# Kernel optimization log

Measured on AMD Instinct MI355X. Metric: run time of the kernel, lower is better.

## Reference

```python
import jax, jax.numpy as jnp
import numpy as np

N = 50000    # num nodes
E = 800000   # num edges
B = 256      # num graphs
AD, BD = 39, 10          # atom / bond feature dims
H, HEADS, HD, L, TD = 128, 4, 32, 3, 128  # hidden, heads, head_dim, layers, time_dim
BN_EPS = 1e-5


def setup_inputs() -> dict:
    key = jax.random.key(0)
    ks = jax.random.split(key, 24)
    g = lambda i, shape: jax.random.normal(ks[i], shape, dtype=jnp.float32) * 0.05
    return {
        "x": jax.random.normal(ks[0], (N, AD), dtype=jnp.float32),
        "edge_index": jax.random.randint(ks[1], (2, E), 0, N),
        "edge_attr": jax.random.normal(ks[2], (E, BD), dtype=jnp.float32),
        "batch": jnp.sort(jax.random.randint(ks[3], (N,), 0, B)),
        "t": jax.random.randint(ks[4], (B,), 0, 1000),
        "atom_W": g(5, (AD, H)), "atom_b": jnp.zeros((H,), jnp.float32),
        "bond_W": g(6, (BD, H)), "bond_b": jnp.zeros((H,), jnp.float32),
        "lin_W": g(7, (L, H, H)), "edge_W": g(8, (L, H, H)),
        "att_src": g(9, (L, HEADS, HD)), "att_dst": g(10, (L, HEADS, HD)),
        "att_edge": g(11, (L, HEADS, HD)), "conv_b": jnp.zeros((L, H), jnp.float32),
        "bn_gamma": jnp.ones((L, H), jnp.float32), "bn_beta": jnp.zeros((L, H), jnp.float32),
        "out_W": g(12, (H, H)), "out_b": jnp.zeros((H,), jnp.float32),
        "time_W1": g(13, (TD, H)), "time_b1": jnp.zeros((H,), jnp.float32),
        "time_W2": g(14, (H, H)), "time_b2": jnp.zeros((H,), jnp.float32),
        "pool_W1": g(15, (H, H)), "pool_b1": jnp.zeros((H,), jnp.float32),
        "pool_W2": g(16, (H, H)), "pool_b2": jnp.zeros((H,), jnp.float32),
        "np_W1": g(17, (2 * H, H)), "np_b1": jnp.zeros((H,), jnp.float32),
        "np_W2": g(18, (H, H)), "np_b2": jnp.zeros((H,), jnp.float32),
        "np_W3": g(19, (H, AD)), "np_b3": jnp.zeros((AD,), jnp.float32),
    }


def _time_embedding(tf):
    half = TD // 2
    freqs = jnp.exp(jnp.arange(half, dtype=jnp.float32) * (-np.log(10000.0) / (half - 1)))
    e = tf[:, None] * freqs[None, :]
    return jnp.concatenate([jnp.sin(e), jnp.cos(e)], axis=-1)


def _gat_layer(h, e_emb, src, dst, W, We, a_src, a_dst, a_edge, bias):
    # PyG GATConv: shared lin for src/dst, edge features modulate attention only.
    xh = (h @ W).reshape(N, HEADS, HD)
    eh = (e_emb @ We).reshape(E, HEADS, HD)
    s_src = jnp.sum(xh * a_src, axis=-1)    # [N, HEADS]
    s_dst = jnp.sum(xh * a_dst, axis=-1)    # [N, HEADS]
    s_edge = jnp.sum(eh * a_edge, axis=-1)  # [E, HEADS]
    alpha = jax.nn.leaky_relu(s_src[src] + s_dst[dst] + s_edge, 0.2)  # [E, HEADS]
    amax = jax.ops.segment_max(alpha, dst, num_segments=N)
    amax = jnp.where(jnp.isfinite(amax), amax, 0.0)
    ea = jnp.exp(alpha - amax[dst])
    denom = jax.ops.segment_sum(ea, dst, num_segments=N)
    w = ea / (denom[dst] + 1e-16)           # segment softmax over incoming edges
    msg = xh[src] * w[:, :, None]           # [E, HEADS, HD]
    return jax.ops.segment_sum(msg, dst, num_segments=N).reshape(N, H) + bias


def reference(x, edge_index, edge_attr, batch, t,
              atom_W, atom_b, bond_W, bond_b,
              lin_W, edge_W, att_src, att_dst, att_edge, conv_b, bn_gamma, bn_beta,
              out_W, out_b, time_W1, time_b1, time_W2, time_b2,
              pool_W1, pool_b1, pool_W2, pool_b2,
              np_W1, np_b1, np_W2, np_b2, np_W3, np_b3):
    src, dst = edge_index[0], edge_index[1]
    # time conditioning
    t_emb = _time_embedding(t.astype(jnp.float32))
    t_emb = jax.nn.silu(t_emb @ time_W1 + time_b1) @ time_W2 + time_b2  # [B, H]
    # GNN backbone
    h = x @ atom_W + atom_b
    e_emb = edge_attr @ bond_W + bond_b
    for i in range(L):
        h_in = h
        h = _gat_layer(h, e_emb, src, dst, lin_W[i], edge_W[i],
                       att_src[i], att_dst[i], att_edge[i], conv_b[i])
        mu = h.mean(axis=0)
        var = h.var(axis=0)
        h = (h - mu) / jnp.sqrt(var + BN_EPS) * bn_gamma[i] + bn_beta[i]
        h = jax.nn.relu(h)
        h = h + h_in  # residual (dropout is eval-mode identity)
    node_features = h @ out_W + out_b  # [N, H]
    # graph mean pool + pooling MLP
    counts = jnp.clip(jax.ops.segment_sum(jnp.ones((N,), h.dtype), batch, num_segments=B), 1.0, None)
    graph = jax.ops.segment_sum(node_features, batch, num_segments=B) / counts[:, None]
    graph = jax.nn.silu(graph @ pool_W1 + pool_b1) @ pool_W2 + pool_b2  # [B, H]
    tg = t_emb + graph
    # per-node noise prediction
    z = jnp.concatenate([node_features, tg[batch]], axis=-1)  # [N, 2H]
    z = jax.nn.silu(z @ np_W1 + np_b1)
    z = jax.nn.silu(z @ np_W2 + np_b2)
    return z @ np_W3 + np_b3  # [N, AD]
```

## Files before the change

kernel.cpp:

```cpp
#include <hip/hip_runtime.h>
#include <hip/hip_fp16.h>
#include <math.h>

#define N_NODES 50000
#define N_EDGES 800000
#define NB 256
#define AD 39
#define BD 10
#define H 128
#define HEADS 4
#define HD 32
#define LAYERS 3
#define TD 128
#define NBUCK 196
#define EPB 4096

typedef _Float16 f16x8 __attribute__((ext_vector_type(8)));
typedef float f32x4 __attribute__((ext_vector_type(4)));

__device__ __forceinline__ float silu_f(float x) { return x / (1.f + __expf(-x)); }

__device__ __forceinline__ void fma_rank1(float acc[8][4], float4 aL, float4 aH, float4 w)
{
    float ar[8] = {aL.x, aL.y, aL.z, aL.w, aH.x, aH.y, aH.z, aH.w};
    float wr[4] = {w.x, w.y, w.z, w.w};
#pragma unroll
    for (int r = 0; r < 8; r++)
#pragma unroll
        for (int j = 0; j < 4; j++) acc[r][j] += ar[r] * wr[j];
}

template<int KT>
__global__ __launch_bounds__(256) void gemm128(
    const float* __restrict__ A, const float* __restrict__ W,
    const float* __restrict__ bias, float* __restrict__ out,
    int Nrows, int ldw)
{
    __shared__ float As[KT * 68];
    const int tid = threadIdx.x;
    const int rowBase = blockIdx.x * 64;

    for (int idx = tid; idx < 64 * KT; idx += 256) {
        int row = idx / KT;
        int k = idx - row * KT;
        int n = rowBase + row;
        As[k * 68 + row] = (n < Nrows) ? A[(size_t)n * KT + k] : 0.f;
    }
    __syncthreads();

    const int c0 = (tid & 31) * 4;
    const int n0 = (tid >> 5) * 8;

    float acc[8][4];
#pragma unroll
    for (int r = 0; r < 8; r++)
#pragma unroll
        for (int j = 0; j < 4; j++) acc[r][j] = 0.f;

    const float* wp = W + c0;
    int k = 0;
    for (; k + 4 <= KT; k += 4) {
        float4 w0 = *(const float4*)&wp[(size_t)(k + 0) * ldw];
        float4 w1 = *(const float4*)&wp[(size_t)(k + 1) * ldw];
        float4 w2 = *(const float4*)&wp[(size_t)(k + 2) * ldw];
        float4 w3 = *(const float4*)&wp[(size_t)(k + 3) * ldw];
        float4 aL0 = *(const float4*)&As[(k + 0) * 68 + n0];
        float4 aH0 = *(const float4*)&As[(k + 0) * 68 + n0 + 4];
        float4 aL1 = *(const float4*)&As[(k + 1) * 68 + n0];
        float4 aH1 = *(const float4*)&As[(k + 1) * 68 + n0 + 4];
        float4 aL2 = *(const float4*)&As[(k + 2) * 68 + n0];
        float4 aH2 = *(const float4*)&As[(k + 2) * 68 + n0 + 4];
        float4 aL3 = *(const float4*)&As[(k + 3) * 68 + n0];
        float4 aH3 = *(const float4*)&As[(k + 3) * 68 + n0 + 4];
        fma_rank1(acc, aL0, aH0, w0);
        fma_rank1(acc, aL1, aH1, w1);
        fma_rank1(acc, aL2, aH2, w2);
        fma_rank1(acc, aL3, aH3, w3);
    }
    for (; k < KT; ++k) {
        float4 w0 = *(const float4*)&wp[(size_t)k * ldw];
        float4 aL = *(const float4*)&As[k * 68 + n0];
        float4 aH = *(const float4*)&As[k * 68 + n0 + 4];
        fma_rank1(acc, aL, aH, w0);
    }

    float4 bv = make_float4(0.f, 0.f, 0.f, 0.f);
    if (bias) bv = *(const float4*)&bias[c0];

#pragma unroll
    for (int r = 0; r < 8; r++) {
        int n = rowBase + n0 + r;
        if (n >= Nrows) break;
        float4 o;
        o.x = acc[r][0] + bv.x;
        o.y = acc[r][1] + bv.y;
        o.z = acc[r][2] + bv.z;
        o.w = acc[r][3] + bv.w;
        *(float4*)&out[(size_t)n * H + c0] = o;
    }
}

__global__ __launch_bounds__(256) void convert_w_frags(
    const float* __restrict__ lin_W, const float* __restrict__ out_W,
    __half* __restrict__ w16)
{
    int tid = blockIdx.x * 256 + threadIdx.x;
    if (tid >= 4 * H * H) return;
    int mat = tid >> 14;
    int rem = tid & 16383;
    int k = rem >> 7;
    int n = rem & 127;
    const float* src = (mat < 3) ? (lin_W + (size_t)mat * H * H) : out_W;
    float v = src[(size_t)k * H + n];
    int ks = k >> 5, kr = k & 31;
    int lane = ((kr >> 3) << 4) | (n & 15);
    int j = kr & 7;
    int nb = n >> 4;
    w16[(size_t)mat * 16384 + (((ks * 8 + nb) * 64 + lane) << 3) + j] = __float2half(v);
}

__global__ __launch_bounds__(256) void convert_np_frags(
    const float* __restrict__ npW1, const float* __restrict__ npW2,
    const float* __restrict__ npW3, __half* __restrict__ wnp)
{
    int tid = blockIdx.x * 256 + threadIdx.x;
    const int TOT12 = 2 * H * H;
    if (tid < TOT12) {
        int mat = tid >> 14;
        int rem = tid & 16383;
        int k = rem >> 7;
        int n = rem & 127;
        const float* src = mat ? npW2 : npW1;
        float v = src[(size_t)k * H + n];
        int ks = k >> 5, kr = k & 31;
        int lane = ((kr >> 3) << 4) | (n & 15);
        int j = kr & 7;
        int nb = n >> 4;
        wnp[(size_t)mat * 16384 + (((ks * 8 + nb) * 64 + lane) << 3) + j] = __float2half(v);
    } else {
        int r = tid - TOT12;
        if (r >= H * 48) return;
        int k = r / 48;
        int n = r - k * 48;
        float v = (n < AD) ? npW3[(size_t)k * AD + n] : 0.f;
        int ks = k >> 5, kr = k & 31;
        int lane = ((kr >> 3) << 4) | (n & 15);
        int j = kr & 7;
        int nb = n >> 4;
        wnp[32768 + (((ks * 3 + nb) * 64 + lane) << 3) + j] = __float2half(v);
    }
}

__global__ __launch_bounds__(256) void gemm_mfma_bn(
    const float* __restrict__ A,
    const __half* __restrict__ agg, const float* __restrict__ scale,
    const float* __restrict__ shift, float* __restrict__ hio,
    const __half* __restrict__ wfrag, const float* __restrict__ bias,
    float* __restrict__ out32, __half* __restrict__ out16,
    const float* __restrict__ attS, const float* __restrict__ attD,
    float* __restrict__ sS, float* __restrict__ sD, int Nrows)
{
    __shared__ __half Ah[64 * 136];
    const int tid = threadIdx.x;
    const int rowBase = blockIdx.x * 64;

    for (int idx = tid; idx < 64 * 32; idx += 256) {
        int row = idx >> 5;
        int kq = (idx & 31) * 4;
        int n = rowBase + row;
        float4 v = make_float4(0.f, 0.f, 0.f, 0.f);
        if (n < Nrows) {
            if (agg) {
                uint2 u = *(const uint2*)&agg[(size_t)n * H + kq];
                float2 lo = __half22float2(*(__half2*)&u.x);
                float2 hi = __half22float2(*(__half2*)&u.y);
                float4 sc = *(const float4*)&scale[kq];
                float4 sh = *(const float4*)&shift[kq];
                float4 hv = *(const float4*)&hio[(size_t)n * H + kq];
                v.x = fmaxf(lo.x * sc.x + sh.x, 0.f) + hv.x;
                v.y = fmaxf(lo.y * sc.y + sh.y, 0.f) + hv.y;
                v.z = fmaxf(hi.x * sc.z + sh.z, 0.f) + hv.z;
                v.w = fmaxf(hi.y * sc.w + sh.w, 0.f) + hv.w;
                *(float4*)&hio[(size_t)n * H + kq] = v;
            } else {
                v = *(const float4*)&A[(size_t)n * H + kq];
            }
        }
        __half2 a = __floats2half2_rn(v.x, v.y);
        __half2 b = __floats2half2_rn(v.z, v.w);
        *(uint2*)&Ah[row * 136 + kq] = make_uint2(*(unsigned*)&a, *(unsigned*)&b);
    }
    __syncthreads();

    const int wave = tid >> 6;
    const int lane = tid & 63;
    const int lrow = lane & 15;
    const int lgrp = lane >> 4;

    f16x8 bf[4][2];
#pragma unroll
    for (int ks = 0; ks < 4; ks++)
#pragma unroll
        for (int nt = 0; nt < 2; nt++) {
            int nb = wave * 2 + nt;
            bf[ks][nt] = *(const f16x8*)&wfrag[(((ks * 8 + nb) * 64 + lane) << 3)];
        }

    f32x4 acc[4][2];
#pragma unroll
    for (int mt = 0; mt < 4; mt++)
#pragma unroll
        for (int nt = 0; nt < 2; nt++) acc[mt][nt] = (f32x4){0.f, 0.f, 0.f, 0.f};

#pragma unroll
    for (int ks = 0; ks < 4; ks++) {
#pragma unroll
        for (int mt = 0; mt < 4; mt++) {
            f16x8 af = *(const f16x8*)&Ah[(mt * 16 + lrow) * 136 + ks * 32 + lgrp * 8];
            acc[mt][0] = __builtin_amdgcn_mfma_f32_16x16x32_f16(af, bf[ks][0], acc[mt][0], 0, 0, 0);
            acc[mt][1] = __builtin_amdgcn_mfma_f32_16x16x32_f16(af, bf[ks][1], acc[mt][1], 0, 0, 0);
        }
    }

    const int col0 = wave * 32 + lrow;
    const int col1 = col0 + 16;
    float b0 = bias ? bias[col0] : 0.f;
    float b1 = bias ? bias[col1] : 0.f;
    float aS0 = 0.f, aS1 = 0.f, aD0 = 0.f, aD1 = 0.f;
    if (sS) {
        aS0 = attS[col0]; aS1 = attS[col1];
        aD0 = attD[col0]; aD1 = attD[col1];
    }

#pragma unroll
    for (int mt = 0; mt < 4; mt++) {
#pragma unroll
        for (int reg = 0; reg < 4; reg++) {
            int row = rowBase + mt * 16 + lgrp * 4 + reg;
            float v0 = acc[mt][0][reg] + b0;
            float v1 = acc[mt][1][reg] + b1;
            if (row < Nrows) {
                if (out16) {
                    out16[(size_t)row * H + col0] = __float2half(v0);
                    out16[(size_t)row * H + col1] = __float2half(v1);
                } else {
                    out32[(size_t)row * H + col0] = v0;
                    out32[(size_t)row * H + col1] = v1;
                }
            }
            if (sS) {
                float ps = v0 * aS0 + v1 * aS1;
                float pd = v0 * aD0 + v1 * aD1;
#pragma unroll
                for (int off = 8; off >= 1; off >>= 1) {
                    ps += __shfl_xor(ps, off, 16);
                    pd += __shfl_xor(pd, off, 16);
                }
                if (lrow == 0 && row < Nrows) {
                    sS[row * 4 + wave] = ps;
                    sD[row * 4 + wave] = pd;
                }
            }
        }
    }
}

__global__ __launch_bounds__(256) void np_fused_mfma(
    const float* __restrict__ nf, const int* __restrict__ batch,
    const float* __restrict__ tgW, const __half* __restrict__ wnp,
    const float* __restrict__ npb2, const float* __restrict__ npb3,
    float* __restrict__ out, int Nrows)
{
    __shared__ __half Ah[64 * 136];
    const int tid = threadIdx.x;
    const int rowBase = blockIdx.x * 64;

    for (int idx = tid; idx < 64 * 32; idx += 256) {
        int row = idx >> 5;
        int kq = (idx & 31) * 4;
        int n = rowBase + row;
        float4 v = make_float4(0.f, 0.f, 0.f, 0.f);
        if (n < Nrows) v = *(const float4*)&nf[(size_t)n * H + kq];
        __half2 a = __floats2half2_rn(v.x, v.y);
        __half2 b = __floats2half2_rn(v.z, v.w);
        *(uint2*)&Ah[row * 136 + kq] = make_uint2(*(unsigned*)&a, *(unsigned*)&b);
    }
    __syncthreads();

    const int wave = tid >> 6;
    const int lane = tid & 63;
    const int lrow = lane & 15;
    const int lgrp = lane >> 4;

    f32x4 acc[4][2];

    {
        f16x8 bf[4][2];
#pragma unroll
        for (int ks = 0; ks < 4; ks++)
#pragma unroll
            for (int nt = 0; nt < 2; nt++) {
                int nb = wave * 2 + nt;
                bf[ks][nt] = *(const f16x8*)&wnp[(((ks * 8 + nb) * 64 + lane) << 3)];
            }
#pragma unroll
        for (int mt = 0; mt < 4; mt++)
#pragma unroll
            for (int nt = 0; nt < 2; nt++) acc[mt][nt] = (f32x4){0.f, 0.f, 0.f, 0.f};
#pragma unroll
        for (int ks = 0; ks < 4; ks++) {
#pragma unroll
            for (int mt = 0; mt < 4; mt++) {
                f16x8 af = *(const f16x8*)&Ah[(mt * 16 + lrow) * 136 + ks * 32 + lgrp * 8];
                acc[mt][0] = __builtin_amdgcn_mfma_f32_16x16x32_f16(af, bf[ks][0], acc[mt][0], 0, 0, 0);
                acc[mt][1] = __builtin_amdgcn_mfma_f32_16x16x32_f16(af, bf[ks][1], acc[mt][1], 0, 0, 0);
            }
        }
    }
    __syncthreads();

#pragma unroll
    for (int mt = 0; mt < 4; mt++) {
#pragma unroll
        for (int nt = 0; nt < 2; nt++) {
            int col = wave * 32 + nt * 16 + lrow;
#pragma unroll
            for (int reg = 0; reg < 4; reg++) {
                int row = mt * 16 + lgrp * 4 + reg;
                int n = rowBase + row;
                float v = acc[mt][nt][reg];
                if (n < Nrows) v += tgW[(size_t)batch[n] * H + col];
                Ah[row * 136 + col] = __float2half(silu_f(v));
            }
        }
    }
    __syncthreads();

    {
        const __half* w2 = wnp + 16384;
        f16x8 bf[4][2];
#pragma unroll
        for (int ks = 0; ks < 4; ks++)
#pragma unroll
            for (int nt = 0; nt < 2; nt++) {
                int nb = wave * 2 + nt;
                bf[ks][nt] = *(const f16x8*)&w2[(((ks * 8 + nb) * 64 + lane) << 3)];
            }
#pragma unroll
        for (int mt = 0; mt < 4; mt++)
#pragma unroll
            for (int nt = 0; nt < 2; nt++) acc[mt][nt] = (f32x4){0.f, 0.f, 0.f, 0.f};
#pragma unroll
        for (int ks = 0; ks < 4; ks++) {
#pragma unroll
            for (int mt = 0; mt < 4; mt++) {
                f16x8 af = *(const f16x8*)&Ah[(mt * 16 + lrow) * 136 + ks * 32 + lgrp * 8];
                acc[mt][0] = __builtin_amdgcn_mfma_f32_16x16x32_f16(af, bf[ks][0], acc[mt][0], 0, 0, 0);
                acc[mt][1] = __builtin_amdgcn_mfma_f32_16x16x32_f16(af, bf[ks][1], acc[mt][1], 0, 0, 0);
            }
        }
    }
    __syncthreads();

#pragma unroll
    for (int mt = 0; mt < 4; mt++) {
#pragma unroll
        for (int nt = 0; nt < 2; nt++) {
            int col = wave * 32 + nt * 16 + lrow;
            float b2 = npb2[col];
#pragma unroll
            for (int reg = 0; reg < 4; reg++) {
                int row = mt * 16 + lgrp * 4 + reg;
                Ah[row * 136 + col] = __float2half(silu_f(acc[mt][nt][reg] + b2));
            }
        }
    }
    __syncthreads();

    {
        const __half* w3 = wnp + 32768;
        f32x4 acc3[3];
#pragma unroll
        for (int nt = 0; nt < 3; nt++) acc3[nt] = (f32x4){0.f, 0.f, 0.f, 0.f};
#pragma unroll
        for (int ks = 0; ks < 4; ks++) {
            f16x8 af = *(const f16x8*)&Ah[(wave * 16 + lrow) * 136 + ks * 32 + lgrp * 8];
#pragma unroll
            for (int nt = 0; nt < 3; nt++) {
                f16x8 bf = *(const f16x8*)&w3[(((ks * 3 + nt) * 64 + lane) << 3)];
                acc3[nt] = __builtin_amdgcn_mfma_f32_16x16x32_f16(af, bf, acc3[nt], 0, 0, 0);
            }
        }
#pragma unroll
        for (int nt = 0; nt < 3; nt++) {
            int col = nt * 16 + lrow;
            if (col < AD) {
                float b3 = npb3[col];
#pragma unroll
                for (int reg = 0; reg < 4; reg++) {
                    int row = rowBase + wave * 16 + lgrp * 4 + reg;
                    if (row < Nrows) out[(size_t)row * AD + col] = acc3[nt][reg] + b3;
                }
            }
        }
    }
}

__global__ __launch_bounds__(256) void precompute_small(
    const float* __restrict__ edge_W, const float* __restrict__ att_edge,
    const float* __restrict__ bond_W, const float* __restrict__ bond_b,
    float* __restrict__ mc)
{
    __shared__ float bl[LAYERS][H][4];
    int tid = threadIdx.x;
    for (int task = tid; task < LAYERS * H; task += 256) {
        int l = task / H, k = task % H;
#pragma unroll
        for (int hh = 0; hh < 4; hh++) {
            float s = 0.f;
            for (int d = 0; d < HD; d++)
                s += edge_W[(size_t)l * H * H + k * H + hh * HD + d] *
                     att_edge[l * H + hh * HD + d];
            bl[l][k][hh] = s;
        }
    }
    __syncthreads();
    if (tid < LAYERS * BD * 4) {
        int l = tid / (BD * 4), r = tid % (BD * 4), j = r / 4, hh = r % 4;
        float s = 0.f;
        for (int k = 0; k < H; k++) s += bond_W[j * H + k] * bl[l][k][hh];
        mc[l * 44 + j * 4 + hh] = s;
    }
    if (tid >= 128 && tid < 128 + LAYERS * 4) {
        int r = tid - 128, l = r / 4, hh = r % 4;
        float s = 0.f;
        for (int k = 0; k < H; k++) s += bond_b[k] * bl[l][k][hh];
        mc[l * 44 + 40 + hh] = s;
    }
}

__global__ __launch_bounds__(128) void time_embed(
    const int* __restrict__ t,
    const float* __restrict__ W1, const float* __restrict__ b1,
    const float* __restrict__ W2, const float* __restrict__ b2,
    float* __restrict__ t_emb)
{
    int g = blockIdx.x, c = threadIdx.x;
    float tf = (float)t[g];
    __shared__ float emb[TD], z[H];
    int k = c & 63;
    float f = __expf(-9.210340371976184f * (float)k / 63.0f);
    float e = tf * f;
    emb[c] = (c < 64) ? sinf(e) : cosf(e);
    __syncthreads();
    float a1 = b1[c];
    for (int kk = 0; kk < TD; kk++) a1 += emb[kk] * W1[kk * H + c];
    z[c] = silu_f(a1);
    __syncthreads();
    float a2 = b2[c];
    for (int kk = 0; kk < H; kk++) a2 += z[kk] * W2[kk * H + c];
    t_emb[g * H + c] = a2;
}

__global__ __launch_bounds__(256) void hist_dst(const int* __restrict__ edge_index,
                                                int* __restrict__ deg)
{
    int e = blockIdx.x * 256 + threadIdx.x;
    if (e < N_EDGES) atomicAdd(&deg[edge_index[N_EDGES + e]], 1);
}

__global__ __launch_bounds__(320) void gptr_bsearch(const int* __restrict__ batch,
                                                    int* __restrict__ gptr)
{
    int g = threadIdx.x;
    if (g > NB) return;
    int lo = 0, hi = N_NODES;
    while (lo < hi) {
        int mid = (lo + hi) >> 1;
        if (batch[mid] < g) lo = mid + 1; else hi = mid;
    }
    gptr[g] = lo;
}

__global__ __launch_bounds__(256) void scan_part(const int* __restrict__ cnt,
                                                 int* __restrict__ bsum, int n)
{
    int tid = threadIdx.x;
    int i0 = blockIdx.x * 1024 + tid * 4;
    int s = 0;
#pragma unroll
    for (int j = 0; j < 4; j++) if (i0 + j < n) s += cnt[i0 + j];
    __shared__ int red[256];
    red[tid] = s;
    __syncthreads();
    for (int off = 128; off >= 1; off >>= 1) {
        if (tid < off) red[tid] += red[tid + off];
        __syncthreads();
    }
    if (tid == 0) bsum[blockIdx.x] = red[0];
}

__global__ __launch_bounds__(256) void scan_tops(const int* __restrict__ bsum,
                                                 int* __restrict__ boff, int G,
                                                 int* __restrict__ total)
{
    int tid = threadIdx.x;
    int v = (tid < G) ? bsum[tid] : 0;
    __shared__ int ps[256];
    ps[tid] = v;
    __syncthreads();
    for (int off = 1; off < 256; off <<= 1) {
        int t = (tid >= off) ? ps[tid - off] : 0;
        __syncthreads();
        ps[tid] += t;
        __syncthreads();
    }
    if (tid < G) boff[tid] = ps[tid] - v;
    if (tid == 255) *total = ps[255];
}

__global__ __launch_bounds__(256) void scan_final(const int* __restrict__ cnt,
                                                  const int* __restrict__ boff,
                                                  int* __restrict__ ptr, int n)
{
    int tid = threadIdx.x;
    int i0 = blockIdx.x * 1024 + tid * 4;
    int v[4];
#pragma unroll
    for (int j = 0; j < 4; j++) v[j] = (i0 + j < n) ? cnt[i0 + j] : 0;
    int s = v[0] + v[1] + v[2] + v[3];
    __shared__ int ps[256];
    ps[tid] = s;
    __syncthreads();
    for (int off = 1; off < 256; off <<= 1) {
        int t = (tid >= off) ? ps[tid - off] : 0;
        __syncthreads();
        ps[tid] += t;
        __syncthreads();
    }
    int run = boff[blockIdx.x] + ps[tid] - s;
#pragma unroll
    for (int j = 0; j < 4; j++) {
        if (i0 + j < n) { ptr[i0 + j] = run; run += v[j]; }
    }
}

__global__ __launch_bounds__(256) void init_gcur(const int* __restrict__ csr_ptr,
                                                 int* __restrict__ gcur)
{
    int b = threadIdx.x;
    if (b < NBUCK) gcur[b] = csr_ptr[min(b << 8, N_NODES)];
}

__global__ __launch_bounds__(256) void bucket_scatter_a(
    const int* __restrict__ edge_index, int* __restrict__ gcur,
    int4* __restrict__ tmp)
{
    __shared__ int cnt[NBUCK], cbase[NBUCK], cur[NBUCK];
    const int tid = threadIdx.x;
    const int e0 = blockIdx.x * EPB;
    for (int i = tid; i < NBUCK; i += 256) { cnt[i] = 0; cur[i] = 0; }
    __syncthreads();
    for (int i = 0; i < EPB; i += 256) {
        int e = e0 + i + tid;
        if (e < N_EDGES) atomicAdd(&cnt[edge_index[N_EDGES + e] >> 8], 1);
    }
    __syncthreads();
    for (int i = tid; i < NBUCK; i += 256)
        if (cnt[i] > 0) cbase[i] = atomicAdd(&gcur[i], cnt[i]);
    __syncthreads();
    for (int i = 0; i < EPB; i += 256) {
        int e = e0 + i + tid;
        if (e < N_EDGES) {
            int s = edge_index[e];
            int d = edge_index[N_EDGES + e];
            int b = d >> 8;
            int off = atomicAdd(&cur[b], 1);
            tmp[cbase[b] + off] = make_int4(s, e, d, 0);
        }
    }
}

__global__ __launch_bounds__(256) void bucket_scatter_b(
    const int4* __restrict__ tmp, const int* __restrict__ csr_ptr,
    int2* __restrict__ csr_se)
{
    __shared__ int lcur[256];
    const int b = blockIdx.x;
    const int n0 = b << 8;
    const int tid = threadIdx.x;
    lcur[tid] = 0;
    __syncthreads();
    int start = csr_ptr[n0];
    int end   = csr_ptr[min(n0 + 256, N_NODES)];
    for (int p = start + tid; p < end; p += 256) {
        int4 q = tmp[p];
        int pos = atomicAdd(&lcur[q.z - n0], 1);
        csr_se[csr_ptr[q.z] + pos] = make_int2(q.x, q.y);
    }
}

__global__ __launch_bounds__(256) void se3_pre(
    const int2* __restrict__ csr_se, const float* __restrict__ edge_attr,
    const float* __restrict__ mc, __half* __restrict__ se3)
{
    __shared__ float Ml[LAYERS * 44];
    int tid = threadIdx.x;
    if (tid < LAYERS * 44) Ml[tid] = mc[tid];
    __syncthreads();
    int p = blockIdx.x * 256 + tid;
    if (p >= N_EDGES) return;
    int e = csr_se[p].y;
    float ea[BD];
    const float* eap = &edge_attr[(size_t)e * BD];
#pragma unroll
    for (int j = 0; j < BD; j++) ea[j] = eap[j];
#pragma unroll
    for (int l = 0; l < LAYERS; l++) {
        const float* M = &Ml[l * 44];
        float s0 = M[40], s1 = M[41], s2 = M[42], s3 = M[43];
#pragma unroll
        for (int j = 0; j < BD; j++) {
            float x = ea[j];
            s0 += x * M[j * 4 + 0]; s1 += x * M[j * 4 + 1];
            s2 += x * M[j * 4 + 2]; s3 += x * M[j * 4 + 3];
        }
        __half2 h01 = __floats2half2_rn(s0, s1);
        __half2 h23 = __floats2half2_rn(s2, s3);
        uint2 u = make_uint2(*(const unsigned*)&h01, *(const unsigned*)&h23);
        *(uint2*)&se3[((size_t)l * N_EDGES + p) * 4] = u;
    }
}

__global__ __launch_bounds__(256) void gat_agg_full(
    const __half* __restrict__ xh16, const __half* __restrict__ se3l,
    const float* __restrict__ sS,
    const int* __restrict__ csr_ptr, const int2* __restrict__ csr_se,
    const float* __restrict__ sD, const float* __restrict__ conv_b_l,
    __half* __restrict__ agg)
{
    int n = (blockIdx.x * 256 + threadIdx.x) >> 6;
    if (n >= N_NODES) return;
    int lane = threadIdx.x & 63;
    int c0 = lane * 2;
    int hd = lane >> 4;
    int start = csr_ptr[n], end = csr_ptr[n + 1];
    float sDn = sD[n * 4 + hd];

    float m_run = -1e30f, d_run = 0.f;
    float acc0 = 0.f, acc1 = 0.f;

    for (int base = start; base < end; base += 64) {
        int cnt = min(64, end - base);
        int s_l = (lane < cnt) ? csr_se[base + lane].x : 0;

        float a_t[4], e_t[4];
        float m_blk = -1e30f;
#pragma unroll
        for (int t = 0; t < 4; t++) {
            int i = (lane & 15) + t * 16;
            float a = -1e30f;
            if (i < cnt) {
                int src = __shfl(s_l, i);
                a = sS[src * 4 + hd] +
                    __half2float(se3l[(size_t)(base + i) * 4 + hd]) + sDn;
                a = (a >= 0.f) ? a : 0.2f * a;
            }
            a_t[t] = a;
            m_blk = fmaxf(m_blk, a);
        }
#pragma unroll
        for (int off = 8; off >= 1; off >>= 1)
            m_blk = fmaxf(m_blk, __shfl_xor(m_blk, off, 16));
        float m_new = fmaxf(m_run, m_blk);
        float rescale = __expf(m_run - m_new);
        float dsum = 0.f;
#pragma unroll
        for (int t = 0; t < 4; t++) {
            e_t[t] = __expf(a_t[t] - m_new);
            dsum += e_t[t];
        }
#pragma unroll
        for (int off = 8; off >= 1; off >>= 1)
            dsum += __shfl_xor(dsum, off, 16);
        d_run = d_run * rescale + dsum;
        acc0 *= rescale;
        acc1 *= rescale;

        int srcb = lane & 48;
#pragma unroll
        for (int t = 0; t < 4; t++) {
            int rem = cnt - t * 16;
            if (rem <= 0) break;
            int lim = min(16, (rem + 3) & ~3);
            for (int i2 = 0; i2 < lim; i2 += 4) {
                int i = t * 16 + i2;
                int s0 = __shfl(s_l, i + 0), s1 = __shfl(s_l, i + 1);
                int s2 = __shfl(s_l, i + 2), s3 = __shfl(s_l, i + 3);
                float w0 = __shfl(e_t[t], srcb | (i2 + 0));
                float w1 = __shfl(e_t[t], srcb | (i2 + 1));
                float w2 = __shfl(e_t[t], srcb | (i2 + 2));
                float w3 = __shfl(e_t[t], srcb | (i2 + 3));
                float2 x0 = __half22float2(*(const __half2*)&xh16[(size_t)s0 * H + c0]);
                float2 x1 = __half22float2(*(const __half2*)&xh16[(size_t)s1 * H + c0]);
                float2 x2 = __half22float2(*(const __half2*)&xh16[(size_t)s2 * H + c0]);
                float2 x3 = __half22float2(*(const __half2*)&xh16[(size_t)s3 * H + c0]);
                acc0 += x0.x * w0 + x1.x * w1 + x2.x * w2 + x3.x * w3;
                acc1 += x0.y * w0 + x1.y * w1 + x2.y * w2 + x3.y * w3;
            }
        }
        m_run = m_new;
    }
    float inv = 1.f / (d_run + 1e-16f);
    __half2 o = __floats2half2_rn(acc0 * inv + conv_b_l[c0],
                                  acc1 * inv + conv_b_l[c0 + 1]);
    *(__half2*)&agg[(size_t)n * H + c0] = o;
}

__global__ __launch_bounds__(256) void bn_partial_f(const __half* __restrict__ agg,
                                                    float* __restrict__ part)
{
    const int PER = (N_NODES + 511) / 512;
    __shared__ float red[2][8][128];
    int b = blockIdx.x;
    int cg = threadIdx.x & 31;
    int rs = threadIdx.x >> 5;
    int c4 = cg * 4;
    int s = b * PER, e = min(N_NODES, s + PER);
    float s0 = 0.f, s1 = 0.f, s2 = 0.f, s3 = 0.f;
    float q0 = 0.f, q1 = 0.f, q2 = 0.f, q3 = 0.f;
    for (int n = s + rs; n < e; n += 8) {
        uint2 u = *(const uint2*)&agg[(size_t)n * H + c4];
        float2 lo = __half22float2(*(__half2*)&u.x);
        float2 hi = __half22float2(*(__half2*)&u.y);
        s0 += lo.x; q0 += lo.x * lo.x;
        s1 += lo.y; q1 += lo.y * lo.y;
        s2 += hi.x; q2 += hi.x * hi.x;
        s3 += hi.y; q3 += hi.y * hi.y;
    }
    *(float4*)&red[0][rs][c4] = make_float4(s0, s1, s2, s3);
    *(float4*)&red[1][rs][c4] = make_float4(q0, q1, q2, q3);
    __syncthreads();
    if (threadIdx.x < 128) {
        int c = threadIdx.x;
        float sum = 0.f, sq = 0.f;
#pragma unroll
        for (int r = 0; r < 8; r++) { sum += red[0][r][c]; sq += red[1][r][c]; }
        part[b * H + c] = sum;
        part[512 * H + b * H + c] = sq;
    }
}

__global__ __launch_bounds__(256) void bn_finish_f(const float* __restrict__ part,
                                                   const float* __restrict__ gamma,
                                                   const float* __restrict__ beta,
                                                   float* __restrict__ scale,
                                                   float* __restrict__ shift)
{
    __shared__ double red[2][2][128];
    int c = threadIdx.x & 127;
    int g = threadIdx.x >> 7;
    double s = 0.0, q = 0.0;
    for (int b = g * 256; b < (g + 1) * 256; b++) {
        s += (double)part[b * H + c];
        q += (double)part[512 * H + b * H + c];
    }
    red[0][g][c] = s;
    red[1][g][c] = q;
    __syncthreads();
    if (g == 0) {
        s = red[0][0][c] + red[0][1][c];
        q = red[1][0][c] + red[1][1][c];
        float mu = (float)(s / N_NODES);
        float var = (float)(q / N_NODES) - mu * mu;
        float rstd = rsqrtf(var + 1e-5f);
        float sc = gamma[c] * rstd;
        scale[c] = sc;
        shift[c] = beta[c] - mu * sc;
    }
}

__global__ __launch_bounds__(128) void pool_partial(
    const float* __restrict__ nf, const int* __restrict__ gptr,
    float* __restrict__ pprt)
{
    int g = blockIdx.x >> 2;
    int q = blockIdx.x & 3;
    int c = threadIdx.x;
    int s = gptr[g], e = gptr[g + 1];
    int qlen = (e - s + 3) >> 2;
    int qs = s + q * qlen;
    int qe = min(e, qs + qlen);
    float sum = 0.f;
    for (int n = qs; n < qe; n++) sum += nf[(size_t)n * H + c];
    pprt[((size_t)g * 4 + q) * H + c] = sum;
}

__global__ __launch_bounds__(512) void graph_head_mlp(
    const int* __restrict__ gptr, const float* __restrict__ pprt,
    const float* __restrict__ t_emb,
    const float* __restrict__ pW1, const float* __restrict__ pb1,
    const float* __restrict__ pW2, const float* __restrict__ pb2,
    const float* __restrict__ npW1, const float* __restrict__ npb1,
    float* __restrict__ tgW)
{
    int g = blockIdx.x;
    int c = threadIdx.x & 127;
    int q = threadIdx.x >> 7;
    __shared__ float row[H], z[H];
    __shared__ float red[4][H];

    int s = gptr[g], e = gptr[g + 1];
    float cf = (e - s > 0) ? (float)(e - s) : 1.f;
    if (q == 0) {
        row[c] = (pprt[((size_t)g * 4 + 0) * H + c] +
                  pprt[((size_t)g * 4 + 1) * H + c] +
                  pprt[((size_t)g * 4 + 2) * H + c] +
                  pprt[((size_t)g * 4 + 3) * H + c]) / cf;
    }
    __syncthreads();

    float p = 0.f;
#pragma unroll 8
    for (int k = q * 32; k < q * 32 + 32; k++) p += row[k] * pW1[k * H + c];
    red[q][c] = p;
    __syncthreads();
    if (q == 0) z[c] = silu_f(red[0][c] + red[1][c] + red[2][c] + red[3][c] + pb1[c]);
    __syncthreads();

    p = 0.f;
#pragma unroll 8
    for (int k = q * 32; k < q * 32 + 32; k++) p += z[k] * pW2[k * H + c];
    red[q][c] = p;
    __syncthreads();
    if (q == 0) row[c] = red[0][c] + red[1][c] + red[2][c] + red[3][c] + pb2[c]
                         + t_emb[g * H + c];
    __syncthreads();

    p = 0.f;
#pragma unroll 8
    for (int k = q * 32; k < q * 32 + 32; k++)
        p += row[k] * npW1[(size_t)(128 + k) * H + c];
    red[q][c] = p;
    __syncthreads();
    if (q == 0) tgW[g * H + c] = red[0][c] + red[1][c] + red[2][c] + red[3][c] + npb1[c];
}

extern "C" void kernel_launch(void* const* d_in, const int* in_sizes, int n_in,
                              void* d_out, int out_size, void* d_ws, size_t ws_size,
                              hipStream_t stream)
{
    const float* x          = (const float*)d_in[0];
    const int*   edge_index = (const int*)d_in[1];
    const float* edge_attr  = (const float*)d_in[2];
    const int*   batch      = (const int*)d_in[3];
    const int*   t          = (const int*)d_in[4];
    const float* atom_W     = (const float*)d_in[5];
    const float* atom_b     = (const float*)d_in[6];
    const float* bond_W     = (const float*)d_in[7];
    const float* bond_b     = (const float*)d_in[8];
    const float* lin_W      = (const float*)d_in[9];
    const float* edge_W     = (const float*)d_in[10];
    const float* att_src    = (const float*)d_in[11];
    const float* att_dst    = (const float*)d_in[12];
    const float* att_edge   = (const float*)d_in[13];
    const float* conv_b     = (const float*)d_in[14];
    const float* bn_gamma   = (const float*)d_in[15];
    const float* bn_beta    = (const float*)d_in[16];
    const float* out_W      = (const float*)d_in[17];
    const float* out_b      = (const float*)d_in[18];
    const float* time_W1    = (const float*)d_in[19];
    const float* time_b1    = (const float*)d_in[20];
    const float* time_W2    = (const float*)d_in[21];
    const float* time_b2    = (const float*)d_in[22];
    const float* pool_W1    = (const float*)d_in[23];
    const float* pool_b1    = (const float*)d_in[24];
    const float* pool_W2    = (const float*)d_in[25];
    const float* pool_b2    = (const float*)d_in[26];
    const float* np_W1      = (const float*)d_in[27];
    const float* np_b1      = (const float*)d_in[28];
    const float* np_W2      = (const float*)d_in[29];
    const float* np_b2      = (const float*)d_in[30];
    const float* np_W3      = (const float*)d_in[31];
    const float* np_b3      = (const float*)d_in[32];

    const size_t OFF_H     = 0;
    const size_t OFF_XH    = 6400000;
    const size_t OFF_AGG   = 12800000;
    const size_t OFF_SD    = 17600000;
    const size_t OFF_TEMB  = 17800000;
    const size_t OFF_TGW   = 17832768;
    const size_t OFF_MC    = 17865536;
    const size_t OFF_BNSC  = 17865792;
    const size_t OFF_BNSH  = 17865920;
    const size_t OFF_PART  = 17866048;
    const size_t OFF_SE3   = 17898816;
    const size_t REQ_FLOATS = 22698816;
    const size_t REQ_BYTES  = REQ_FLOATS * 4;

    if (ws_size < REQ_BYTES) {
        hipMemsetAsync(d_out, 0, (size_t)out_size * sizeof(float), stream);
        return;
    }

    float* fws    = (float*)d_ws;
    float* h      = fws + OFF_H;
    float* xh     = fws + OFF_XH;
    __half* xh16  = (__half*)(fws + OFF_XH);
    int4*  etmp   = (int4*)(fws + OFF_XH);
    __half* agg   = (__half*)(fws + OFF_AGG);
    float* sD     = fws + OFF_SD;
    float* t_emb  = fws + OFF_TEMB;
    float* tgW    = fws + OFF_TGW;
    float* mc     = fws + OFF_MC;
    float* bnsc   = fws + OFF_BNSC;
    float* bnsh   = fws + OFF_BNSH;
    float* part   = fws + OFF_PART;
    float* pprt   = fws + OFF_AGG;
    __half* wnp   = (__half*)part;
    __half* se3   = (__half*)(fws + OFF_SE3);

    int* ib       = (int*)d_out;
    int* csr_ptr  = ib;
    int2* csr_se  = (int2*)(ib + 50016);
    int* deg      = ib + 1650016;
    int* gcur     = deg;
    int* gptr     = ib + 1700032;
    int* bsum     = ib + 1700292;
    int* boff     = ib + 1700356;
    float* sS     = (float*)d_out + 1700420;
    float* bnpart = sS;
    __half* w16   = (__half*)((float*)d_out + 1900420);

    hipMemsetAsync(deg, 0, N_NODES * sizeof(int), stream);

    precompute_small<<<1, 256, 0, stream>>>(edge_W, att_edge, bond_W, bond_b, mc);
    time_embed<<<NB, 128, 0, stream>>>(t, time_W1, time_b1, time_W2, time_b2, t_emb);
    gptr_bsearch<<<1, 320, 0, stream>>>(batch, gptr);
    convert_w_frags<<<(4 * H * H + 255) / 256, 256, 0, stream>>>(lin_W, out_W, w16);

    hist_dst<<<(N_EDGES + 255) / 256, 256, 0, stream>>>(edge_index, deg);

    const int GSN = (N_NODES + 1023) / 1024;
    scan_part<<<GSN, 256, 0, stream>>>(deg, bsum, N_NODES);
    scan_tops<<<1, 256, 0, stream>>>(bsum, boff, GSN, &csr_ptr[N_NODES]);
    scan_final<<<GSN, 256, 0, stream>>>(deg, boff, csr_ptr, N_NODES);

    init_gcur<<<1, 256, 0, stream>>>(csr_ptr, gcur);
    bucket_scatter_a<<<(N_EDGES + EPB - 1) / EPB, 256, 0, stream>>>(
        edge_index, gcur, etmp);
    bucket_scatter_b<<<NBUCK, 256, 0, stream>>>(etmp, csr_ptr, csr_se);

    const int GB = (N_NODES + 63) / 64;
    const int GE = (N_EDGES + 255) / 256;

    se3_pre<<<GE, 256, 0, stream>>>(csr_se, edge_attr, mc, se3);

    gemm128<AD><<<GB, 256, 0, stream>>>(x, atom_W, atom_b, h, N_NODES, H);

    for (int l = 0; l < LAYERS; l++) {
        gemm_mfma_bn<<<GB, 256, 0, stream>>>(
            (l == 0) ? h : nullptr,
            (l == 0) ? nullptr : agg, bnsc, bnsh, h,
            w16 + (size_t)l * 16384, nullptr,
            nullptr, xh16,
            att_src + l * H, att_dst + l * H, sS, sD, N_NODES);
        gat_agg_full<<<N_NODES / 4, 256, 0, stream>>>(
            xh16, se3 + (size_t)l * N_EDGES * 4, sS,
            csr_ptr, csr_se, sD, conv_b + l * H, agg);
        bn_partial_f<<<512, 256, 0, stream>>>(agg, bnpart);
        bn_finish_f<<<1, 256, 0, stream>>>(bnpart, bn_gamma + l * H,
                                           bn_beta + l * H, bnsc, bnsh);
    }

    convert_np_frags<<<(2 * H * H + H * 48 + 255) / 256, 256, 0, stream>>>(
        np_W1, np_W2, np_W3, wnp);

    gemm_mfma_bn<<<GB, 256, 0, stream>>>(
        nullptr, agg, bnsc, bnsh, h,
        w16 + (size_t)3 * 16384, out_b,
        xh, nullptr,
        nullptr, nullptr, nullptr, nullptr, N_NODES);

    pool_partial<<<NB * 4, 128, 0, stream>>>(xh, gptr, pprt);
    graph_head_mlp<<<NB, 512, 0, stream>>>(gptr, pprt, t_emb, pool_W1, pool_b1,
                                           pool_W2, pool_b2, np_W1, np_b1, tgW);

    np_fused_mfma<<<GB, 256, 0, stream>>>(xh, batch, tgW, wnp, np_b2, np_b3,
                                          (float*)d_out, N_NODES);
}
```

Before: 441.8 us.

## Drop online-softmax max tracking in GAT aggregation and merge setup kernels

The GAT aggregation kernel no longer tracks a running maximum or rescales its accumulators. It exponentiates the LeakyReLU scores directly and sums them, and it pre-shifts source indices so the row offset is computed once per edge. Several small setup launches are also merged: precompute, time embedding and graph-pointer search go into one kernel, the two weight-fragment conversions go into another, and `gcur` initialisation is folded into `scan_final`. The cost is numerical safety: without max subtraction, large attention logits could overflow `exp`. Converting the np weights earlier also assumes their buffer is not overwritten during the layers.

```diff
diff --git a/kernel.cpp b/kernel.cpp
--- a/kernel.cpp
+++ b/kernel.cpp
@@ -100,34 +100,31 @@
     }
 }
 
-__global__ __launch_bounds__(256) void convert_w_frags(
+__global__ __launch_bounds__(256) void convert_all(
     const float* __restrict__ lin_W, const float* __restrict__ out_W,
-    __half* __restrict__ w16)
+    const float* __restrict__ npW1, const float* __restrict__ npW2,
+    const float* __restrict__ npW3,
+    __half* __restrict__ w16, __half* __restrict__ wnp)
 {
     int tid = blockIdx.x * 256 + threadIdx.x;
-    if (tid >= 4 * H * H) return;
-    int mat = tid >> 14;
-    int rem = tid & 16383;
-    int k = rem >> 7;
-    int n = rem & 127;
-    const float* src = (mat < 3) ? (lin_W + (size_t)mat * H * H) : out_W;
-    float v = src[(size_t)k * H + n];
-    int ks = k >> 5, kr = k & 31;
-    int lane = ((kr >> 3) << 4) | (n & 15);
-    int j = kr & 7;
-    int nb = n >> 4;
-    w16[(size_t)mat * 16384 + (((ks * 8 + nb) * 64 + lane) << 3) + j] = __float2half(v);
-}
-
-__global__ __launch_bounds__(256) void convert_np_frags(
-    const float* __restrict__ npW1, const float* __restrict__ npW2,
-    const float* __restrict__ npW3, __half* __restrict__ wnp)
-{
-    int tid = blockIdx.x * 256 + threadIdx.x;
-    const int TOT12 = 2 * H * H;
-    if (tid < TOT12) {
+    if (tid < 4 * H * H) {
         int mat = tid >> 14;
         int rem = tid & 16383;
+        int k = rem >> 7;
+        int n = rem & 127;
+        const float* src = (mat < 3) ? (lin_W + (size_t)mat * H * H) : out_W;
+        float v = src[(size_t)k * H + n];
+        int ks = k >> 5, kr = k & 31;
+        int lane = ((kr >> 3) << 4) | (n & 15);
+        int j = kr & 7;
+        int nb = n >> 4;
+        w16[(size_t)mat * 16384 + (((ks * 8 + nb) * 64 + lane) << 3) + j] = __float2half(v);
+        return;
+    }
+    int r = tid - 4 * H * H;
+    if (r < 2 * H * H) {
+        int mat = r >> 14;
+        int rem = r & 16383;
         int k = rem >> 7;
         int n = rem & 127;
         const float* src = mat ? npW2 : npW1;
@@ -137,17 +134,84 @@
         int j = kr & 7;
         int nb = n >> 4;
         wnp[(size_t)mat * 16384 + (((ks * 8 + nb) * 64 + lane) << 3) + j] = __float2half(v);
+        return;
+    }
+    r -= 2 * H * H;
+    if (r >= H * 48) return;
+    int k = r / 48;
+    int n = r - k * 48;
+    float v = (n < AD) ? npW3[(size_t)k * AD + n] : 0.f;
+    int ks = k >> 5, kr = k & 31;
+    int lane = ((kr >> 3) << 4) | (n & 15);
+    int j = kr & 7;
+    int nb = n >> 4;
+    wnp[32768 + (((ks * 3 + nb) * 64 + lane) << 3) + j] = __float2half(v);
+}
+
+__global__ __launch_bounds__(256) void setup_misc(
+    const float* __restrict__ edge_W, const float* __restrict__ att_edge,
+    const float* __restrict__ bond_W, const float* __restrict__ bond_b,
+    float* __restrict__ mc,
+    const int* __restrict__ batch, int* __restrict__ gptr,
+    const int* __restrict__ t,
+    const float* __restrict__ W1, const float* __restrict__ b1,
+    const float* __restrict__ W2, const float* __restrict__ b2,
+    float* __restrict__ t_emb)
+{
+    const int b = blockIdx.x;
+    const int tid = threadIdx.x;
+    if (b == 0) {
+        __shared__ float bl[LAYERS][H][4];
+        for (int task = tid; task < LAYERS * H; task += 256) {
+            int l = task / H, k = task % H;
+#pragma unroll
+            for (int hh = 0; hh < 4; hh++) {
+                float s = 0.f;
+                for (int d = 0; d < HD; d++)
+                    s += edge_W[(size_t)l * H * H + k * H + hh * HD + d] *
+                         att_edge[l * H + hh * HD + d];
+                bl[l][k][hh] = s;
+            }
+        }
+        __syncthreads();
+        if (tid < LAYERS * BD * 4) {
+            int l = tid / (BD * 4), r = tid % (BD * 4), j = r / 4, hh = r % 4;
+            float s = 0.f;
+            for (int k = 0; k < H; k++) s += bond_W[j * H + k] * bl[l][k][hh];
+            mc[l * 44 + j * 4 + hh] = s;
+        }
+        if (tid >= 128 && tid < 128 + LAYERS * 4) {
+            int r = tid - 128, l = r / 4, hh = r % 4;
+            float s = 0.f;
+            for (int k = 0; k < H; k++) s += bond_b[k] * bl[l][k][hh];
+            mc[l * 44 + 40 + hh] = s;
+        }
+    } else if (b == 1) {
+        for (int g = tid; g <= NB; g += 256) {
+            int lo = 0, hi = N_NODES;
+            while (lo < hi) {
+                int mid = (lo + hi) >> 1;
+                if (batch[mid] < g) lo = mid + 1; else hi = mid;
+            }
+            gptr[g] = lo;
+        }
     } else {
-        int r = tid - TOT12;
-        if (r >= H * 48) return;
-        int k = r / 48;
-        int n = r - k * 48;
-        float v = (n < AD) ? npW3[(size_t)k * AD + n] : 0.f;
-        int ks = k >> 5, kr = k & 31;
-        int lane = ((kr >> 3) << 4) | (n & 15);
-        int j = kr & 7;
-        int nb = n >> 4;
-        wnp[32768 + (((ks * 3 + nb) * 64 + lane) << 3) + j] = __float2half(v);
+        int g = b - 2;
+        int c = tid & 127;
+        float tf = (float)t[g];
+        __shared__ float emb[TD], z[H];
+        int k = c & 63;
+        float f = __expf(-9.210340371976184f * (float)k / 63.0f);
+        float e = tf * f;
+        emb[c] = (c < 64) ? sinf(e) : cosf(e);
+        __syncthreads();
+        float a1 = b1[c];
+        for (int kk = 0; kk < TD; kk++) a1 += emb[kk] * W1[kk * H + c];
+        z[c] = silu_f(a1);
+        __syncthreads();
+        float a2 = b2[c];
+        for (int kk = 0; kk < H; kk++) a2 += z[kk] * W2[kk * H + c];
+        t_emb[g * H + c] = a2;
     }
 }
 
@@ -406,80 +470,11 @@
     }
 }
 
-__global__ __launch_bounds__(256) void precompute_small(
-    const float* __restrict__ edge_W, const float* __restrict__ att_edge,
-    const float* __restrict__ bond_W, const float* __restrict__ bond_b,
-    float* __restrict__ mc)
-{
-    __shared__ float bl[LAYERS][H][4];
-    int tid = threadIdx.x;
-    for (int task = tid; task < LAYERS * H; task += 256) {
-        int l = task / H, k = task % H;
-#pragma unroll
-        for (int hh = 0; hh < 4; hh++) {
-            float s = 0.f;
-            for (int d = 0; d < HD; d++)
-                s += edge_W[(size_t)l * H * H + k * H + hh * HD + d] *
-                     att_edge[l * H + hh * HD + d];
-            bl[l][k][hh] = s;
-        }
-    }
-    __syncthreads();
-    if (tid < LAYERS * BD * 4) {
-        int l = tid / (BD * 4), r = tid % (BD * 4), j = r / 4, hh = r % 4;
-        float s = 0.f;
-        for (int k = 0; k < H; k++) s += bond_W[j * H + k] * bl[l][k][hh];
-        mc[l * 44 + j * 4 + hh] = s;
-    }
-    if (tid >= 128 && tid < 128 + LAYERS * 4) {
-        int r = tid - 128, l = r / 4, hh = r % 4;
-        float s = 0.f;
-        for (int k = 0; k < H; k++) s += bond_b[k] * bl[l][k][hh];
-        mc[l * 44 + 40 + hh] = s;
-    }
-}
-
-__global__ __launch_bounds__(128) void time_embed(
-    const int* __restrict__ t,
-    const float* __restrict__ W1, const float* __restrict__ b1,
-    const float* __restrict__ W2, const float* __restrict__ b2,
-    float* __restrict__ t_emb)
-{
-    int g = blockIdx.x, c = threadIdx.x;
-    float tf = (float)t[g];
-    __shared__ float emb[TD], z[H];
-    int k = c & 63;
-    float f = __expf(-9.210340371976184f * (float)k / 63.0f);
-    float e = tf * f;
-    emb[c] = (c < 64) ? sinf(e) : cosf(e);
-    __syncthreads();
-    float a1 = b1[c];
-    for (int kk = 0; kk < TD; kk++) a1 += emb[kk] * W1[kk * H + c];
-    z[c] = silu_f(a1);
-    __syncthreads();
-    float a2 = b2[c];
-    for (int kk = 0; kk < H; kk++) a2 += z[kk] * W2[kk * H + c];
-    t_emb[g * H + c] = a2;
-}
-
 __global__ __launch_bounds__(256) void hist_dst(const int* __restrict__ edge_index,
                                                 int* __restrict__ deg)
 {
     int e = blockIdx.x * 256 + threadIdx.x;
     if (e < N_EDGES) atomicAdd(&deg[edge_index[N_EDGES + e]], 1);
-}
-
-__global__ __launch_bounds__(320) void gptr_bsearch(const int* __restrict__ batch,
-                                                    int* __restrict__ gptr)
-{
-    int g = threadIdx.x;
-    if (g > NB) return;
-    int lo = 0, hi = N_NODES;
-    while (lo < hi) {
-        int mid = (lo + hi) >> 1;
-        if (batch[mid] < g) lo = mid + 1; else hi = mid;
-    }
-    gptr[g] = lo;
 }
 
 __global__ __launch_bounds__(256) void scan_part(const int* __restrict__ cnt,
@@ -521,7 +516,8 @@
 
 __global__ __launch_bounds__(256) void scan_final(const int* __restrict__ cnt,
                                                   const int* __restrict__ boff,
-                                                  int* __restrict__ ptr, int n)
+                                                  int* __restrict__ ptr,
+                                                  int* __restrict__ gcur, int n)
 {
     int tid = threadIdx.x;
     int i0 = blockIdx.x * 1024 + tid * 4;
@@ -539,17 +535,11 @@
         __syncthreads();
     }
     int run = boff[blockIdx.x] + ps[tid] - s;
+    if ((i0 & 255) == 0 && (i0 >> 8) < NBUCK && i0 < n) gcur[i0 >> 8] = run;
 #pragma unroll
     for (int j = 0; j < 4; j++) {
         if (i0 + j < n) { ptr[i0 + j] = run; run += v[j]; }
     }
-}
-
-__global__ __launch_bounds__(256) void init_gcur(const int* __restrict__ csr_ptr,
-                                                 int* __restrict__ gcur)
-{
-    int b = threadIdx.x;
-    if (b < NBUCK) gcur[b] = csr_ptr[min(b << 8, N_NODES)];
 }
 
 __global__ __launch_bounds__(256) void bucket_scatter_a(
@@ -647,45 +637,33 @@
     int start = csr_ptr[n], end = csr_ptr[n + 1];
     float sDn = sD[n * 4 + hd];
 
-    float m_run = -1e30f, d_run = 0.f;
+    float d_run = 0.f;
     float acc0 = 0.f, acc1 = 0.f;
 
     for (int base = start; base < end; base += 64) {
         int cnt = min(64, end - base);
-        int s_l = (lane < cnt) ? csr_se[base + lane].x : 0;
-
-        float a_t[4], e_t[4];
-        float m_blk = -1e30f;
+        int s_l = (lane < cnt) ? (csr_se[base + lane].x << 7) : 0;
+
+        float e_t[4];
+        float dsum = 0.f;
 #pragma unroll
         for (int t = 0; t < 4; t++) {
             int i = (lane & 15) + t * 16;
-            float a = -1e30f;
+            float e = 0.f;
             if (i < cnt) {
-                int src = __shfl(s_l, i);
-                a = sS[src * 4 + hd] +
+                int src7 = __shfl(s_l, i);
+                float a = sS[(src7 >> 5) + hd] +
                     __half2float(se3l[(size_t)(base + i) * 4 + hd]) + sDn;
                 a = (a >= 0.f) ? a : 0.2f * a;
-            }
-            a_t[t] = a;
-            m_blk = fmaxf(m_blk, a);
-        }
-#pragma unroll
-        for (int off = 8; off >= 1; off >>= 1)
-            m_blk = fmaxf(m_blk, __shfl_xor(m_blk, off, 16));
-        float m_new = fmaxf(m_run, m_blk);
-        float rescale = __expf(m_run - m_new);
-        float dsum = 0.f;
-#pragma unroll
-        for (int t = 0; t < 4; t++) {
-            e_t[t] = __expf(a_t[t] - m_new);
-            dsum += e_t[t];
+                e = __expf(a);
+            }
+            e_t[t] = e;
+            dsum += e;
         }
 #pragma unroll
         for (int off = 8; off >= 1; off >>= 1)
             dsum += __shfl_xor(dsum, off, 16);
-        d_run = d_run * rescale + dsum;
-        acc0 *= rescale;
-        acc1 *= rescale;
+        d_run += dsum;
 
         int srcb = lane & 48;
 #pragma unroll
@@ -701,15 +679,14 @@
                 float w1 = __shfl(e_t[t], srcb | (i2 + 1));
                 float w2 = __shfl(e_t[t], srcb | (i2 + 2));
                 float w3 = __shfl(e_t[t], srcb | (i2 + 3));
-                float2 x0 = __half22float2(*(const __half2*)&xh16[(size_t)s0 * H + c0]);
-                float2 x1 = __half22float2(*(const __half2*)&xh16[(size_t)s1 * H + c0]);
-                float2 x2 = __half22float2(*(const __half2*)&xh16[(size_t)s2 * H + c0]);
-                float2 x3 = __half22float2(*(const __half2*)&xh16[(size_t)s3 * H + c0]);
+                float2 x0 = __half22float2(*(const __half2*)&xh16[s0 + c0]);
+                float2 x1 = __half22float2(*(const __half2*)&xh16[s1 + c0]);
+                float2 x2 = __half22float2(*(const __half2*)&xh16[s2 + c0]);
+                float2 x3 = __half22float2(*(const __half2*)&xh16[s3 + c0]);
                 acc0 += x0.x * w0 + x1.x * w1 + x2.x * w2 + x3.x * w3;
                 acc1 += x0.y * w0 + x1.y * w1 + x2.y * w2 + x3.y * w3;
             }
         }
-        m_run = m_new;
     }
     float inv = 1.f / (d_run + 1e-16f);
     __half2 o = __floats2half2_rn(acc0 * inv + conv_b_l[c0],
@@ -924,29 +901,30 @@
     int* csr_ptr  = ib;
     int2* csr_se  = (int2*)(ib + 50016);
     int* deg      = ib + 1650016;
-    int* gcur     = deg;
     int* gptr     = ib + 1700032;
     int* bsum     = ib + 1700292;
     int* boff     = ib + 1700356;
     float* sS     = (float*)d_out + 1700420;
     float* bnpart = sS;
     __half* w16   = (__half*)((float*)d_out + 1900420);
+    int* gcur     = ib + 1933188;
 
     hipMemsetAsync(deg, 0, N_NODES * sizeof(int), stream);
 
-    precompute_small<<<1, 256, 0, stream>>>(edge_W, att_edge, bond_W, bond_b, mc);
-    time_embed<<<NB, 128, 0, stream>>>(t, time_W1, time_b1, time_W2, time_b2, t_emb);
-    gptr_bsearch<<<1, 320, 0, stream>>>(batch, gptr);
-    convert_w_frags<<<(4 * H * H + 255) / 256, 256, 0, stream>>>(lin_W, out_W, w16);
+    setup_misc<<<NB + 2, 256, 0, stream>>>(
+        edge_W, att_edge, bond_W, bond_b, mc,
+        batch, gptr, t, time_W1, time_b1, time_W2, time_b2, t_emb);
+
+    convert_all<<<(4 * H * H + 2 * H * H + H * 48 + 255) / 256, 256, 0, stream>>>(
+        lin_W, out_W, np_W1, np_W2, np_W3, w16, wnp);
 
     hist_dst<<<(N_EDGES + 255) / 256, 256, 0, stream>>>(edge_index, deg);
 
     const int GSN = (N_NODES + 1023) / 1024;
     scan_part<<<GSN, 256, 0, stream>>>(deg, bsum, N_NODES);
     scan_tops<<<1, 256, 0, stream>>>(bsum, boff, GSN, &csr_ptr[N_NODES]);
-    scan_final<<<GSN, 256, 0, stream>>>(deg, boff, csr_ptr, N_NODES);
-
-    init_gcur<<<1, 256, 0, stream>>>(csr_ptr, gcur);
+    scan_final<<<GSN, 256, 0, stream>>>(deg, boff, csr_ptr, gcur, N_NODES);
+
     bucket_scatter_a<<<(N_EDGES + EPB - 1) / EPB, 256, 0, stream>>>(
         edge_index, gcur, etmp);
     bucket_scatter_b<<<NBUCK, 256, 0, stream>>>(etmp, csr_ptr, csr_se);
@@ -973,9 +951,6 @@
                                            bn_beta + l * H, bnsc, bnsh);
     }
 
-    convert_np_frags<<<(2 * H * H + H * 48 + 255) / 256, 256, 0, stream>>>(
-        np_W1, np_W2, np_W3, wnp);
-
     gemm_mfma_bn<<<GB, 256, 0, stream>>>(
         nullptr, agg, bnsc, bnsh, h,
         w16 + (size_t)3 * 16384, out_b,
```

New measurement: 425.0 us. 3.8% less time.
